# Performance work log

Measured on AMD Instinct MI355X. Metric: run time of the kernel, lower is better.

Reference implementation:

```python
import jax, jax.numpy as jnp
import numpy as np

# Model dims (match init_kwargs)
N_HEADS = 32
N_KV_HEADS = 8
DIM = 4096
HEAD_DIM = DIM // N_HEADS  # 128
N_REP = N_HEADS // N_KV_HEADS  # 4
MAX_SEQ_LEN = 2048
THETA = 10000.0


def precompute_freqs(dim, end, theta=THETA):
    inv = 1.0 / (theta ** (jnp.arange(0, dim, 2, dtype=jnp.float32) / dim))  # [dim/2]
    t = jnp.arange(end, dtype=jnp.float32)
    f = jnp.outer(t, inv)  # [end, dim/2]
    return jnp.cos(f), jnp.sin(f)


def apply_rope(x, cos, sin):
    # x: [b, s, h, d]; cos/sin: [s, d/2]. Pairs (x[...,2i], x[...,2i+1]) form complex numbers.
    xr = x[..., 0::2]
    xi = x[..., 1::2]
    c = cos[None, :, None, :]
    s = sin[None, :, None, :]
    out_r = xr * c - xi * s
    out_i = xr * s + xi * c
    return jnp.stack([out_r, out_i], axis=-1).reshape(x.shape)


def setup_inputs() -> dict:
    key = jax.random.key(0)
    ks = jax.random.split(key, 5)
    B, S = 4, 1024
    x = jax.random.normal(ks[0], (B, S, DIM), dtype=jnp.float32)
    wq = jax.random.normal(ks[1], (DIM, N_HEADS * HEAD_DIM), dtype=jnp.float32) * 0.02
    wk = jax.random.normal(ks[2], (DIM, N_KV_HEADS * HEAD_DIM), dtype=jnp.float32) * 0.02
    wv = jax.random.normal(ks[3], (DIM, N_KV_HEADS * HEAD_DIM), dtype=jnp.float32) * 0.02
    wo = jax.random.normal(ks[4], (N_HEADS * HEAD_DIM, DIM), dtype=jnp.float32) * 0.02
    # causal mask, additive: 0 on/below diagonal, -1e9 above
    mask = jnp.where(jnp.tril(jnp.ones((S, S), dtype=bool)), 0.0, -1e9).astype(jnp.float32)[None, None]
    return {"x": x, "wq": wq, "wk": wk, "wv": wv, "wo": wo, "mask": mask, "start_pos": 0}


def reference(x, wq, wk, wv, wo, mask, start_pos):
    B, S, _ = x.shape
    # QKV projections
    xq = (x @ wq).reshape(B, S, N_HEADS, HEAD_DIM)
    xk = (x @ wk).reshape(B, S, N_KV_HEADS, HEAD_DIM)
    xv = (x @ wv).reshape(B, S, N_KV_HEADS, HEAD_DIM)
    # RoPE on q, k at positions [start_pos, start_pos+S)
    cos, sin = precompute_freqs(HEAD_DIM, MAX_SEQ_LEN * 2)
    cos_s = jax.lax.dynamic_slice_in_dim(cos, start_pos, S, 0)
    sin_s = jax.lax.dynamic_slice_in_dim(sin, start_pos, S, 0)
    xq = apply_rope(xq, cos_s, sin_s)
    xk = apply_rope(xk, cos_s, sin_s)
    # KV-cache scatter-update (cache starts zeroed), then read prefix
    cache_k = jnp.zeros((B, MAX_SEQ_LEN, N_KV_HEADS, HEAD_DIM), dtype=x.dtype)
    cache_v = jnp.zeros_like(cache_k)
    cache_k = jax.lax.dynamic_update_slice(cache_k, xk, (0, start_pos, 0, 0))
    cache_v = jax.lax.dynamic_update_slice(cache_v, xv, (0, start_pos, 0, 0))
    kv_len = start_pos + S
    keys = cache_k[:, :kv_len]    # [b, kv_len, n_kv, d]
    values = cache_v[:, :kv_len]
    # GQA without materializing repeated KV: split q heads into (kv_group, rep)
    q = xq.reshape(B, S, N_KV_HEADS, N_REP, HEAD_DIM)
    scale = 1.0 / jnp.sqrt(jnp.float32(HEAD_DIM)).astype(x.dtype)
    scores = jnp.einsum('bsgrd,btgd->bgrst', q, keys) * scale  # [b, g, r, s, t]
    scores = scores + mask.reshape(1, 1, 1, S, kv_len)
    probs = jax.nn.softmax(scores, axis=-1)
    out = jnp.einsum('bgrst,btgd->bsgrd', probs, values)  # [b, s, g, r, d]
    out = out.reshape(B, S, N_HEADS * HEAD_DIM)
    return out @ wo
```

## Files before the change

### kernel.cpp

```cpp
#include <hip/hip_runtime.h>
#include <hip/hip_bf16.h>
#include <stdint.h>

typedef __bf16 bf16raw;
typedef __attribute__((ext_vector_type(8))) __bf16 bf16x8;
typedef __attribute__((ext_vector_type(4))) float f32x4;

#define DIMD 4096
#define NHEAD 32
#define NKVH 8
#define HD 128
#define SEQ 1024
#define NB 4
#define NTOK 4096
#define NQKV 6144

__device__ __forceinline__ void gload_lds16(const void* gsrc, void* ldst) {
  __builtin_amdgcn_global_load_lds(
      (const __attribute__((address_space(1))) void*)gsrc,
      (__attribute__((address_space(3))) void*)ldst, 16, 0, 0);
}

__global__ void cast_f32_bf16_kernel(const float* __restrict__ src,
                                     __hip_bfloat16* __restrict__ dst, int n) {
  int i = (blockIdx.x * 256 + threadIdx.x) * 8;
  if (i >= n) return;
  f32x4 a = *(const f32x4*)(src + i);
  f32x4 b = *(const f32x4*)(src + i + 4);
  union { bf16x8 v; __hip_bfloat16 e[8]; } o;
#pragma unroll
  for (int j = 0; j < 4; ++j) {
    o.e[j] = __float2bfloat16(a[j]);
    o.e[4 + j] = __float2bfloat16(b[j]);
  }
  *(bf16x8*)(dst + i) = o.v;
}

__global__ void transpose_cast_kernel(const float* __restrict__ src,
                                      __hip_bfloat16* __restrict__ dst,
                                      int K, int N) {
  __shared__ float tile[32][33];
  int n0 = blockIdx.x * 32, k0 = blockIdx.y * 32;
  int tx = threadIdx.x, ty = threadIdx.y;
#pragma unroll
  for (int i = 0; i < 4; ++i)
    tile[ty + 8 * i][tx] = src[(size_t)(k0 + ty + 8 * i) * N + n0 + tx];
  __syncthreads();
#pragma unroll
  for (int i = 0; i < 4; ++i)
    dst[(size_t)(n0 + ty + 8 * i) * K + k0 + tx] =
        __float2bfloat16(tile[tx][ty + 8 * i]);
}

__global__ void rope_table_kernel(float* __restrict__ cosb, float* __restrict__ sinb) {
  int idx = blockIdx.x * 256 + threadIdx.x;
  int s = idx >> 6, j = idx & 63;
  float inv = 1.0f / powf(10000.0f, (float)(2 * j) * (1.0f / 128.0f));
  float ang = (float)s * inv;
  cosb[idx] = cosf(ang);
  sinb[idx] = sinf(ang);
}

__global__ void rope_apply_kernel(__hip_bfloat16* __restrict__ qkv,
                                  const float* __restrict__ cosb,
                                  const float* __restrict__ sinb) {
  int idx = blockIdx.x * 256 + threadIdx.x;
  int u = idx & 15;
  int th = idx >> 4;
  int h = th % 40;
  int t = th / 40;
  int s = t & (SEQ - 1);
  int col = (h < 32) ? h * HD : DIMD + (h - 32) * HD;
  __hip_bfloat16* p = qkv + (size_t)t * NQKV + col + u * 8;
  union { bf16x8 v; __hip_bfloat16 e[8]; } x, o;
  x.v = *(const bf16x8*)p;
  const float* cb = cosb + s * 64 + u * 4;
  const float* sb = sinb + s * 64 + u * 4;
#pragma unroll
  for (int e2 = 0; e2 < 4; ++e2) {
    float xr = __bfloat162float(x.e[2 * e2]);
    float xi = __bfloat162float(x.e[2 * e2 + 1]);
    float c = cb[e2], sn = sb[e2];
    o.e[2 * e2] = __float2bfloat16(xr * c - xi * sn);
    o.e[2 * e2 + 1] = __float2bfloat16(xr * sn + xi * c);
  }
  *(bf16x8*)p = o.v;
}

__global__ void v_transpose_kernel(const __hip_bfloat16* __restrict__ qkv,
                                   __hip_bfloat16* __restrict__ vt) {
  __shared__ __hip_bfloat16 tile[32][33];
  int bh = blockIdx.x;
  int s0 = blockIdx.y * 32;
  int d0 = blockIdx.z * 32;
  int b = bh >> 3, h = bh & 7;
  int tx = threadIdx.x, ty = threadIdx.y;
  const __hip_bfloat16* src =
      qkv + (size_t)(b * SEQ) * NQKV + DIMD + NKVH * HD + h * HD;
#pragma unroll
  for (int i = 0; i < 4; ++i)
    tile[ty + 8 * i][tx] = src[(size_t)(s0 + ty + 8 * i) * NQKV + d0 + tx];
  __syncthreads();
  int tIdx = s0 >> 6;
  int sLow = s0 & 32;
  __hip_bfloat16* dst = vt + ((size_t)bh * 16 + tIdx) * (128 * 64);
#pragma unroll
  for (int i = 0; i < 4; ++i)
    dst[(size_t)(d0 + ty + 8 * i) * 64 + sLow + tx] = tile[tx][ty + 8 * i];
}


#define PH_SYNC_PRE()                                \
  __builtin_amdgcn_s_barrier();                      \
  asm volatile("s_waitcnt lgkmcnt(0)" ::: "memory"); \
  __builtin_amdgcn_sched_barrier(0);                 \
  __builtin_amdgcn_s_setprio(1)

#define PH_SYNC_POST()            \
  __builtin_amdgcn_s_setprio(0);  \
  __builtin_amdgcn_s_barrier()

#define QMFMA(AFR, BFR, MB, NB)                                            \
  _Pragma("unroll") for (int mf2 = 0; mf2 < 4; ++mf2)                      \
  _Pragma("unroll") for (int nf2 = 0; nf2 < 2; ++nf2)                      \
  _Pragma("unroll") for (int kk2 = 0; kk2 < 2; ++kk2)                      \
      acc[(MB) + mf2][(NB) + nf2] = __builtin_amdgcn_mfma_f32_16x16x32_bf16( \
          AFR[mf2 * 2 + kk2], BFR[nf2 * 2 + kk2], acc[(MB) + mf2][(NB) + nf2], 0, 0, 0)

#define TILE4(BUF, ST1, ST2, ST3, ST4, VM)                        \
  {                                                               \
    _Pragma("unroll") for (int mf = 0; mf < 4; ++mf)              \
    _Pragma("unroll") for (int kk = 0; kk < 2; ++kk)              \
        alo[mf * 2 + kk] = ldsA(BUF, mf, kk);                     \
    _Pragma("unroll") for (int nf = 0; nf < 2; ++nf)              \
    _Pragma("unroll") for (int kk = 0; kk < 2; ++kk)              \
        bq[nf * 2 + kk] = ldsB(BUF, nf, kk);                      \
    ST1;                                                          \
    PH_SYNC_PRE();                                                \
    QMFMA(alo, bq, 0, 0);                                         \
    PH_SYNC_POST();                                               \
    _Pragma("unroll") for (int mf = 0; mf < 4; ++mf)              \
    _Pragma("unroll") for (int kk = 0; kk < 2; ++kk)              \
        ahi[mf * 2 + kk] = ldsA(BUF, mf + 4, kk);                 \
    ST2;                                                          \
    PH_SYNC_PRE();                                                \
    QMFMA(ahi, bq, 4, 0);                                         \
    PH_SYNC_POST();                                               \
    _Pragma("unroll") for (int nf = 0; nf < 2; ++nf)              \
    _Pragma("unroll") for (int kk = 0; kk < 2; ++kk)              \
        bq[nf * 2 + kk] = ldsB(BUF, nf + 2, kk);                  \
    ST3;                                                          \
    PH_SYNC_PRE();                                                \
    QMFMA(alo, bq, 0, 2);                                         \
    PH_SYNC_POST();                                               \
    ST4;                                                          \
    PH_SYNC_PRE();                                                \
    QMFMA(ahi, bq, 4, 2);                                         \
    __builtin_amdgcn_s_setprio(0);                                \
    VM;                                                           \
    __builtin_amdgcn_s_barrier();                                 \
  }

template <typename OutT>
__global__ __launch_bounds__(512, 2) void gemm256_kernel(
    const __hip_bfloat16* __restrict__ A, const __hip_bfloat16* __restrict__ BT,
    OutT* __restrict__ C, int M, int N, int K) {
  __shared__ __align__(16) char lds_[131072];
  const int tid = threadIdx.x;
  const int w = tid >> 6, l = tid & 63;
  const int lr = l & 15, lk = l >> 4;
  const int wm = w >> 2, wn = w & 3;

  const int nbn = N >> 8;
  const int nwg = (M >> 8) * nbn;
  const int cpx = nwg >> 3;
  const int bid = blockIdx.x;
  const int swz = (bid & 7) * cpx + (bid >> 3);
  const int m0 = (swz / nbn) << 8;
  const int n0 = (swz % nbn) << 8;

  const size_t Kb = (size_t)K * 2;
  const char* Ab = (const char*)A + (size_t)m0 * Kb;
  const char* Bb = (const char*)BT + (size_t)n0 * Kb;
  const int srcb = ((l & 7) ^ (l >> 3)) * 16;
  const int crow = l >> 3;

  auto stageA = [&](int buf, int half, int kt) {
#pragma unroll
    for (int j = 0; j < 2; ++j) {
      int row = half * 128 + (w * 2 + j) * 8 + crow;
      gload_lds16(Ab + (size_t)row * Kb + (size_t)kt * 128 + srcb,
                  lds_ + buf * 65536 + half * 16384 + (w * 2 + j) * 1024);
    }
  };
  auto stageB = [&](int buf, int half, int kt) {
#pragma unroll
    for (int j = 0; j < 2; ++j) {
      int row = half * 128 + (w * 2 + j) * 8 + crow;
      gload_lds16(Bb + (size_t)row * Kb + (size_t)kt * 128 + srcb,
                  lds_ + buf * 65536 + 32768 + half * 16384 + (w * 2 + j) * 1024);
    }
  };
  auto ldsA = [&](int buf, int mf, int kk) {
    int rih = mf * 16 + lr;
    int cb = (kk * 64 + lk * 16) ^ ((lr & 7) << 4);
    return *(const bf16x8*)(lds_ + buf * 65536 + wm * 16384 + rih * 128 + cb);
  };
  auto ldsB = [&](int buf, int nf, int kk) {
    int rih = (wn & 1) * 64 + nf * 16 + lr;
    int cb = (kk * 64 + lk * 16) ^ ((lr & 7) << 4);
    return *(const bf16x8*)(lds_ + buf * 65536 + 32768 + (wn >> 1) * 16384 +
                            rih * 128 + cb);
  };

  f32x4 acc[8][4] = {};
  bf16x8 alo[8], ahi[8], bq[4];

  stageA(0, 0, 0);
  stageA(0, 1, 0);
  stageB(0, 0, 0);
  stageB(0, 1, 0);
  stageA(1, 0, 1);
  stageA(1, 1, 1);
  asm volatile("s_waitcnt vmcnt(4)" ::: "memory");
  __builtin_amdgcn_s_barrier();

  const int NT = K >> 6;
  const int nit = (NT >> 1) - 1;
  for (int i = 0; i < nit; ++i) {
    const int E = 2 * i;
    TILE4(0, stageB(1, 0, E + 1), stageB(1, 1, E + 1),
          stageA(0, 0, E + 2), stageA(0, 1, E + 2),
          asm volatile("s_waitcnt vmcnt(4)" ::: "memory"));
    TILE4(1, stageB(0, 0, E + 2), stageB(0, 1, E + 2),
          stageA(1, 0, E + 3), stageA(1, 1, E + 3),
          asm volatile("s_waitcnt vmcnt(4)" ::: "memory"));
  }
  TILE4(0, stageB(1, 0, NT - 1), stageB(1, 1, NT - 1), (void)0, (void)0,
        asm volatile("s_waitcnt vmcnt(0)" ::: "memory"));
  TILE4(1, (void)0, (void)0, (void)0, (void)0, (void)0);

#pragma unroll
  for (int mf = 0; mf < 8; ++mf) {
    int row = m0 + wm * 128 + mf * 16 + lk * 4;
#pragma unroll
    for (int nf = 0; nf < 4; ++nf) {
      int col = n0 + wn * 64 + nf * 16 + lr;
#pragma unroll
      for (int j = 0; j < 4; ++j) {
        size_t off = (size_t)(row + j) * N + col;
        if constexpr (sizeof(OutT) == 2)
          C[off] = __float2bfloat16(acc[mf][nf][j]);
        else
          C[off] = acc[mf][nf][j];
      }
    }
  }
}

__global__ __launch_bounds__(256, 2) void attn_kernel(
    const __hip_bfloat16* __restrict__ qkv,
    const __hip_bfloat16* __restrict__ vtc,
    __hip_bfloat16* __restrict__ out) {
  __shared__ __align__(16) char Ks[2][16384];
  __shared__ __align__(16) char Vs[2][16384];
  __shared__ __align__(16) char Ps[4][2048];

  const int tid = threadIdx.x;
  const int w = tid >> 6, l = tid & 63;
  const int lr = l & 15, lk = l >> 4;
  const int bx = blockIdx.x;
  const int pair = bx >> 7;
  const int hb = bx & 127;
  const int h = hb & 31;
  const int b = hb >> 5;
  const int hk = h >> 2;

  const char* KgB = (const char*)qkv +
                    ((size_t)(b * SEQ) * NQKV + DIMD + hk * HD) * 2;
  const char* VgB = (const char*)vtc + (size_t)(b * NKVH + hk) * (16 * 16384);
  char* Pw = &Ps[w][0];

  const float scale = 0.08838834764831845f;

  auto stageK = [&](int buf, int kvb) {
#pragma unroll
    for (int j = 0; j < 4; ++j) {
      int i = w * 4 + j;
      int row = i * 4 + (l >> 4);
      int si = ((l & 15) * 16) ^ ((row & 7) << 4);
      gload_lds16(KgB + (size_t)(kvb + row) * (NQKV * 2) + si,
                  &Ks[buf][i * 1024]);
    }
  };
  auto stageV = [&](int buf, int t) {
#pragma unroll
    for (int j = 0; j < 4; ++j) {
      int i = w * 4 + j;
      int row = i * 8 + (l >> 3);
      int si = ((l & 7) * 16) ^ ((row & 7) << 4);
      gload_lds16(VgB + (size_t)t * 16384 + row * 128 + si,
                  &Vs[buf][i * 1024]);
    }
  };

  for (int qsel = 0; qsel < 2; ++qsel) {
    const int qtile = qsel ? (15 - pair) : pair;
    const int qbase = qtile * 64 + w * 16;
    const int nkv = qtile + 1;

    const __hip_bfloat16* Qp =
        qkv + (size_t)(b * SEQ + qbase + lr) * NQKV + h * HD + lk * 8;
    bf16x8 aq[4];
#pragma unroll
    for (int ks = 0; ks < 4; ++ks) aq[ks] = *(const bf16x8*)(Qp + ks * 32);

    f32x4 O[8] = {};
    float m_run[4], lsum[4];
#pragma unroll
    for (int j = 0; j < 4; ++j) { m_run[j] = -3.0e38f; lsum[j] = 0.f; }

    stageK(0, 0);
    stageV(0, 0);
    asm volatile("s_waitcnt vmcnt(0)" ::: "memory");
    __syncthreads();

    for (int t = 0; t < nkv; ++t) {
      const int cur = t & 1;
      if (t + 1 < nkv) {
        stageK(cur ^ 1, (t + 1) * 64);
        stageV(cur ^ 1, t + 1);
      }
      const int kvb = t * 64;

      f32x4 st[4] = {};
      __builtin_amdgcn_s_setprio(1);
#pragma unroll
      for (int nt = 0; nt < 4; ++nt) {
        int row = nt * 16 + lr;
        const char* kr = &Ks[cur][row * 256];
        int sw = (row & 7) << 4;
#pragma unroll
        for (int ks = 0; ks < 4; ++ks) {
          bf16x8 bk = *(const bf16x8*)(kr + ((ks * 64 + lk * 16) ^ sw));
          st[nt] = __builtin_amdgcn_mfma_f32_16x16x32_bf16(aq[ks], bk, st[nt], 0, 0, 0);
        }
      }
      __builtin_amdgcn_s_setprio(0);

      const bool needmask = (kvb + 63 > qbase);
      float sv[4][4];
      float tmax[4];
#pragma unroll
      for (int j = 0; j < 4; ++j) {
        int qrow = qbase + lk * 4 + j;
        float mx = -3.0e38f;
#pragma unroll
        for (int nt = 0; nt < 4; ++nt) {
          float v = st[nt][j] * scale;
          if (needmask && (kvb + nt * 16 + lr > qrow)) v = -3.0e38f;
          sv[j][nt] = v;
          mx = fmaxf(mx, v);
        }
        mx = fmaxf(mx, __shfl_xor(mx, 1));
        mx = fmaxf(mx, __shfl_xor(mx, 2));
        mx = fmaxf(mx, __shfl_xor(mx, 4));
        mx = fmaxf(mx, __shfl_xor(mx, 8));
        tmax[j] = mx;
      }
      float corr[4];
#pragma unroll
      for (int j = 0; j < 4; ++j) {
        float mn = fmaxf(m_run[j], tmax[j]);
        corr[j] = __expf(m_run[j] - mn);
        m_run[j] = mn;
      }
#pragma unroll
      for (int j = 0; j < 4; ++j) {
        float rs = 0.f;
        int prow = lk * 4 + j;
        int sw = (prow & 7) << 4;
#pragma unroll
        for (int nt = 0; nt < 4; ++nt) {
          float p = __expf(sv[j][nt] - m_run[j]);
          rs += p;
          *(__hip_bfloat16*)(Pw + prow * 128 + (((nt * 16 + lr) * 2) ^ sw)) =
              __float2bfloat16(p);
        }
        rs += __shfl_xor(rs, 1);
        rs += __shfl_xor(rs, 2);
        rs += __shfl_xor(rs, 4);
        rs += __shfl_xor(rs, 8);
        lsum[j] = lsum[j] * corr[j] + rs;
      }
#pragma unroll
      for (int dt = 0; dt < 8; ++dt)
#pragma unroll
        for (int j = 0; j < 4; ++j) O[dt][j] *= corr[j];

      asm volatile("s_waitcnt lgkmcnt(0)" ::: "memory");
      __builtin_amdgcn_sched_barrier(0);

      __builtin_amdgcn_s_setprio(1);
#pragma unroll
      for (int ks = 0; ks < 2; ++ks) {
        bf16x8 ap = *(const bf16x8*)(Pw + lr * 128 +
                                     ((ks * 64 + lk * 16) ^ ((lr & 7) << 4)));
#pragma unroll
        for (int dt = 0; dt < 8; ++dt) {
          int row = dt * 16 + lr;
          bf16x8 bv = *(const bf16x8*)(&Vs[cur][row * 128 +
                                               ((ks * 64 + lk * 16) ^ ((row & 7) << 4))]);
          O[dt] = __builtin_amdgcn_mfma_f32_16x16x32_bf16(ap, bv, O[dt], 0, 0, 0);
        }
      }
      __builtin_amdgcn_s_setprio(0);

      __syncthreads();
    }

#pragma unroll
    for (int j = 0; j < 4; ++j) {
      float inv = 1.0f / lsum[j];
      __hip_bfloat16* orow =
          out + (size_t)(b * SEQ + qbase + lk * 4 + j) * DIMD + h * HD;
#pragma unroll
      for (int dt = 0; dt < 8; ++dt)
        orow[dt * 16 + lr] = __float2bfloat16(O[dt][j] * inv);
    }
  }
}

extern "C" void kernel_launch(void* const* d_in, const int* in_sizes, int n_in,
                              void* d_out, int out_size, void* d_ws, size_t ws_size,
                              hipStream_t stream) {
  const float* x = (const float*)d_in[0];
  const float* wq = (const float*)d_in[1];
  const float* wk = (const float*)d_in[2];
  const float* wv = (const float*)d_in[3];
  const float* wo = (const float*)d_in[4];
  float* out = (float*)d_out;

  char* ws = (char*)d_ws;
  const size_t MB = 1024 * 1024;
  __hip_bfloat16* xb = (__hip_bfloat16*)(ws);
  __hip_bfloat16* wqkvt = (__hip_bfloat16*)(ws + 32 * MB);
  __hip_bfloat16* wot = (__hip_bfloat16*)(ws + 80 * MB);
  __hip_bfloat16* qkv = (__hip_bfloat16*)(ws + 112 * MB);
  __hip_bfloat16* vtc = (__hip_bfloat16*)(ws + 160 * MB);
  float* cosb = (float*)(ws + 168 * MB);
  float* sinb = cosb + SEQ * 64;

  cast_f32_bf16_kernel<<<NTOK * DIMD / 8 / 256, 256, 0, stream>>>(x, xb, NTOK * DIMD);
  transpose_cast_kernel<<<dim3(128, 128), dim3(32, 8), 0, stream>>>(wq, wqkvt, 4096, 4096);
  transpose_cast_kernel<<<dim3(32, 128), dim3(32, 8), 0, stream>>>(
      wk, wqkvt + (size_t)4096 * 4096, 4096, 1024);
  transpose_cast_kernel<<<dim3(32, 128), dim3(32, 8), 0, stream>>>(
      wv, wqkvt + (size_t)5120 * 4096, 4096, 1024);
  transpose_cast_kernel<<<dim3(128, 128), dim3(32, 8), 0, stream>>>(wo, wot, 4096, 4096);
  rope_table_kernel<<<SEQ * 64 / 256, 256, 0, stream>>>(cosb, sinb);
  gemm256_kernel<__hip_bfloat16><<<dim3(384), 512, 0, stream>>>(
      xb, wqkvt, qkv, NTOK, NQKV, DIMD);
  rope_apply_kernel<<<NTOK * 40 * 16 / 256, 256, 0, stream>>>(qkv, cosb, sinb);
  v_transpose_kernel<<<dim3(32, 32, 4), dim3(32, 8), 0, stream>>>(qkv, vtc);
  attn_kernel<<<dim3(1024), 256, 0, stream>>>(qkv, vtc, xb);
  gemm256_kernel<float><<<dim3(256), 512, 0, stream>>>(
      xb, wot, out, NTOK, DIMD, DIMD);
}
```

Measured before the change: 523.1 us.

## Restage GEMM pipeline to prefetch full A/B tiles into the same buffer

Reworks the double-buffered LDS pipeline of the 256x256 GEMM so that both A and B for tile t+2 are staged into the buffer currently being consumed, issued after the last LDS reads of that buffer. The prologue now preloads both tiles fully and the steady-state waits on vmcnt(8) instead of 4, which keeps more global loads in flight. It also adds a partial lgkmcnt wait before the first MFMA phase. The risk is a write-after-read hazard on the same LDS buffer if other waves are still reading it, which the barriers in PH_PRE must cover.

```diff
diff --git a/kernel.cpp b/kernel.cpp
--- a/kernel.cpp
+++ b/kernel.cpp
@@ -110,13 +110,13 @@
 }
 
 
-#define PH_SYNC_PRE()                                \
+#define PH_PRE()                                     \
   __builtin_amdgcn_s_barrier();                      \
   asm volatile("s_waitcnt lgkmcnt(0)" ::: "memory"); \
   __builtin_amdgcn_sched_barrier(0);                 \
   __builtin_amdgcn_s_setprio(1)
 
-#define PH_SYNC_POST()            \
+#define PH_POST()                 \
   __builtin_amdgcn_s_setprio(0);  \
   __builtin_amdgcn_s_barrier()
 
@@ -127,7 +127,7 @@
       acc[(MB) + mf2][(NB) + nf2] = __builtin_amdgcn_mfma_f32_16x16x32_bf16( \
           AFR[mf2 * 2 + kk2], BFR[nf2 * 2 + kk2], acc[(MB) + mf2][(NB) + nf2], 0, 0, 0)
 
-#define TILE4(BUF, ST1, ST2, ST3, ST4, VM)                        \
+#define TILE(BUF, KT2, DOSTAGE, VMN)                              \
   {                                                               \
     _Pragma("unroll") for (int mf = 0; mf < 4; ++mf)              \
     _Pragma("unroll") for (int kk = 0; kk < 2; ++kk)              \
@@ -135,29 +135,28 @@
     _Pragma("unroll") for (int nf = 0; nf < 2; ++nf)              \
     _Pragma("unroll") for (int kk = 0; kk < 2; ++kk)              \
         bq[nf * 2 + kk] = ldsB(BUF, nf, kk);                      \
-    ST1;                                                          \
-    PH_SYNC_PRE();                                                \
+    asm volatile("s_waitcnt lgkmcnt(8)" ::: "memory");            \
+    PH_PRE();                                                     \
     QMFMA(alo, bq, 0, 0);                                         \
-    PH_SYNC_POST();                                               \
+    PH_POST();                                                    \
     _Pragma("unroll") for (int mf = 0; mf < 4; ++mf)              \
     _Pragma("unroll") for (int kk = 0; kk < 2; ++kk)              \
         ahi[mf * 2 + kk] = ldsA(BUF, mf + 4, kk);                 \
-    ST2;                                                          \
-    PH_SYNC_PRE();                                                \
+    PH_PRE();                                                     \
     QMFMA(ahi, bq, 4, 0);                                         \
-    PH_SYNC_POST();                                               \
+    PH_POST();                                                    \
     _Pragma("unroll") for (int nf = 0; nf < 2; ++nf)              \
     _Pragma("unroll") for (int kk = 0; kk < 2; ++kk)              \
         bq[nf * 2 + kk] = ldsB(BUF, nf + 2, kk);                  \
-    ST3;                                                          \
-    PH_SYNC_PRE();                                                \
+    if (DOSTAGE) { stageA(BUF, 0, KT2); stageA(BUF, 1, KT2); }    \
+    PH_PRE();                                                     \
     QMFMA(alo, bq, 0, 2);                                         \
-    PH_SYNC_POST();                                               \
-    ST4;                                                          \
-    PH_SYNC_PRE();                                                \
+    PH_POST();                                                    \
+    if (DOSTAGE) { stageB(BUF, 0, KT2); stageB(BUF, 1, KT2); }    \
+    PH_PRE();                                                     \
     QMFMA(ahi, bq, 4, 2);                                         \
     __builtin_amdgcn_s_setprio(0);                                \
-    VM;                                                           \
+    asm volatile("s_waitcnt vmcnt(" #VMN ")" ::: "memory");       \
     __builtin_amdgcn_s_barrier();                                 \
   }
 
@@ -222,23 +221,18 @@
   stageB(0, 1, 0);
   stageA(1, 0, 1);
   stageA(1, 1, 1);
-  asm volatile("s_waitcnt vmcnt(4)" ::: "memory");
+  stageB(1, 0, 1);
+  stageB(1, 1, 1);
+  asm volatile("s_waitcnt vmcnt(8)" ::: "memory");
   __builtin_amdgcn_s_barrier();
 
   const int NT = K >> 6;
-  const int nit = (NT >> 1) - 1;
-  for (int i = 0; i < nit; ++i) {
-    const int E = 2 * i;
-    TILE4(0, stageB(1, 0, E + 1), stageB(1, 1, E + 1),
-          stageA(0, 0, E + 2), stageA(0, 1, E + 2),
-          asm volatile("s_waitcnt vmcnt(4)" ::: "memory"));
-    TILE4(1, stageB(0, 0, E + 2), stageB(0, 1, E + 2),
-          stageA(1, 0, E + 3), stageA(1, 1, E + 3),
-          asm volatile("s_waitcnt vmcnt(4)" ::: "memory"));
-  }
-  TILE4(0, stageB(1, 0, NT - 1), stageB(1, 1, NT - 1), (void)0, (void)0,
-        asm volatile("s_waitcnt vmcnt(0)" ::: "memory"));
-  TILE4(1, (void)0, (void)0, (void)0, (void)0, (void)0);
+  for (int t = 0; t < NT - 2; t += 2) {
+    TILE(0, t + 2, true, 8);
+    TILE(1, t + 3, true, 8);
+  }
+  TILE(0, 0, false, 0);
+  TILE(1, 0, false, 0);
 
 #pragma unroll
   for (int mf = 0; mf < 8; ++mf) {
```

New measurement: 532.5 us. Within noise of the previous version (+1.8%).
